# Performance work log

Measured on AMD Instinct MI355X. Metric: run time of the kernel, lower is better.

Reference implementation:

```python
import jax, jax.numpy as jnp
import numpy as np

D_MODEL = 512
N_HEADS = 8
D_HEAD = D_MODEL // N_HEADS
B = 8
N = 1024
EPS = 1e-5  # torch LayerNorm default


def setup_inputs() -> dict:
    key = jax.random.key(0)
    ks = jax.random.split(key, 12)
    x = jax.random.normal(ks[0], (B, N, D_MODEL), dtype=jnp.float32)
    adj = (jax.random.uniform(ks[1], (B, N, N)) < 0.05).astype(jnp.float32)
    s = 1.0 / np.sqrt(D_MODEL)
    def lin(kw, kb):
        W = jax.random.uniform(kw, (D_MODEL, D_MODEL), minval=-s, maxval=s, dtype=jnp.float32)
        b = jax.random.uniform(kb, (D_MODEL,), minval=-s, maxval=s, dtype=jnp.float32)
        return W, b
    Wq, bq = lin(ks[2], ks[3])
    Wk, bk = lin(ks[4], ks[5])
    Wv, bv = lin(ks[6], ks[7])
    Wo, bo = lin(ks[8], ks[9])
    gamma = jnp.ones((D_MODEL,), dtype=jnp.float32)
    beta = jnp.zeros((D_MODEL,), dtype=jnp.float32)
    return {"x": x, "adj": adj, "Wq": Wq, "bq": bq, "Wk": Wk, "bk": bk,
            "Wv": Wv, "bv": bv, "Wo": Wo, "bo": bo, "gamma": gamma, "beta": beta}


def reference(x, adj, Wq, bq, Wk, bk, Wv, bv, Wo, bo, gamma, beta):
    Bsz, n, _ = x.shape
    # QKV projections -> [b, h, n, d]
    def proj(W, b):
        y = x @ W.T + b
        return y.reshape(Bsz, n, N_HEADS, D_HEAD).transpose(0, 2, 1, 3)
    q, k, v = proj(Wq, bq), proj(Wk, bk), proj(Wv, bv)
    scores = jnp.einsum('bhqd,bhkd->bhqk', q, k) / np.sqrt(D_HEAD)
    # adjacency mask + self-loops, broadcast over heads
    mask = (adj + jnp.eye(n, dtype=adj.dtype)[None]) > 0  # [b, n, n]
    scores = jnp.where(mask[:, None], scores, -jnp.inf)
    attn = jax.nn.softmax(scores, axis=-1)  # dropout is identity in eval
    out = jnp.einsum('bhqk,bhkd->bhqd', attn, v)
    out = out.transpose(0, 2, 1, 3).reshape(Bsz, n, D_MODEL)
    out = out @ Wo.T + bo
    # residual + LayerNorm
    h = x + out
    mu = jnp.mean(h, axis=-1, keepdims=True)
    var = jnp.mean(jnp.square(h - mu), axis=-1, keepdims=True)
    return (h - mu) * jax.lax.rsqrt(var + EPS) * gamma + beta
```

## Files before the change

kernel.cpp:

```cpp
#include <hip/hip_runtime.h>

typedef __bf16 bf16;
typedef bf16 bf16x8 __attribute__((ext_vector_type(8)));
typedef bf16 bf16x4 __attribute__((ext_vector_type(4)));
typedef float f32x4 __attribute__((ext_vector_type(4)));
typedef unsigned long long u64;

#define B_SZ 8
#define N_SEQ 1024
#define DMODEL 512
#define N_HEADS 8
#define D_HEAD 64
#define M_ROWS 8192

static constexpr size_t OFF_XB   = 0;
static constexpr size_t OFF_WQKV = (size_t)M_ROWS * DMODEL * 2;
static constexpr size_t OFF_WO   = OFF_WQKV + (size_t)1536 * 512 * 2;
static constexpr size_t OFF_BQKV = OFF_WO + (size_t)512 * 512 * 2;
static constexpr size_t OFF_Q    = OFF_BQKV + 1536 * 4;
static constexpr size_t OFF_K    = OFF_Q + (size_t)64 * 1024 * 64 * 2;
static constexpr size_t OFF_V    = OFF_K + (size_t)64 * 1024 * 64 * 2;
static constexpr size_t OFF_MASK = OFF_V + (size_t)64 * 1024 * 64 * 2;

#define PREP_X_BLK 4096
#define PREP_W_BLK 4102
#define PREP_M_BLK 32768

__device__ __forceinline__ f32x4 mfma16(bf16x8 a, bf16x8 b, f32x4 c) {
  return __builtin_amdgcn_mfma_f32_16x16x32_bf16(a, b, c, 0, 0, 0);
}

__device__ __forceinline__ int sidx(int row, int col) {
  return (row << 6) + (col ^ ((row & 7) << 3));
}

__device__ __forceinline__ void gload16(const void* g, void* l) {
  __builtin_amdgcn_global_load_lds(
      (const __attribute__((address_space(1))) void*)g,
      (__attribute__((address_space(3))) void*)l, 16, 0, 0);
}

__global__ void k_prep(const float* __restrict__ x, const float* __restrict__ adj,
                       const float* __restrict__ Wq, const float* __restrict__ Wk,
                       const float* __restrict__ Wv, const float* __restrict__ Wo,
                       const float* __restrict__ bq, const float* __restrict__ bk,
                       const float* __restrict__ bv,
                       bf16* __restrict__ xb, bf16* __restrict__ wqkv,
                       bf16* __restrict__ wo, float* __restrict__ bqkv,
                       u64* __restrict__ maskb) {
  int b = blockIdx.x;
  if (b < PREP_X_BLK) {
    int i = b * 256 + threadIdx.x;
    float4 v = reinterpret_cast<const float4*>(x)[i];
    bf16x4 o = { (bf16)v.x, (bf16)v.y, (bf16)v.z, (bf16)v.w };
    *reinterpret_cast<bf16x4*>(xb + (size_t)i * 4) = o;
  } else if (b < PREP_X_BLK + PREP_W_BLK) {
    int tid = (b - PREP_X_BLK) * 256 + threadIdx.x;
    if (tid < 1536 * 512) {
      int row = tid >> 9;
      const float* Wsrc = row < 512 ? Wq : row < 1024 ? Wk : Wv;
      wqkv[tid] = (bf16)Wsrc[((row & 511) << 9) | (tid & 511)];
    } else if (tid < 1536 * 512 + 512 * 512) {
      int t = tid - 1536 * 512;
      wo[t] = (bf16)Wo[t];
    } else if (tid < 1536 * 512 + 512 * 512 + 1536) {
      int t = tid - (1536 * 512 + 512 * 512);
      bqkv[t] = t < 512 ? bq[t] : t < 1024 ? bk[t - 512] : bv[t - 1024];
    }
  } else {
    int idx = (b - (PREP_X_BLK + PREP_W_BLK)) * 256 + threadIdx.x;
    int q = (idx >> 10) & 1023, k = idx & 1023;
    bool pred = (adj[idx] > 0.f) || (q == k);
    u64 bal = __ballot(pred);
    if ((threadIdx.x & 63) == 0) maskb[idx >> 6] = bal;
  }
}

__global__ __launch_bounds__(256) void k_gemm(const bf16* __restrict__ A,
    const bf16* __restrict__ W, int ncols, int mode,
    const float* __restrict__ bias, const float* __restrict__ xres,
    bf16* __restrict__ oq, bf16* __restrict__ okk, bf16* __restrict__ ov,
    float* __restrict__ oh) {
  __shared__ bf16 Al[128 * 64];
  __shared__ bf16 Bl[128 * 64];
  int nbx = ncols >> 7;
  int bx = blockIdx.x % nbx, by = blockIdx.x / nbx;
  int m0 = by << 7, n0 = bx << 7;
  int tid = threadIdx.x, lane = tid & 63, w = tid >> 6;
  int wr = (w >> 1) << 6, wc = (w & 1) << 6;
  int lrow = lane & 15, lg = lane >> 4, lko = lg * 8;
  int rl = lane >> 3;
  int csw = ((lane & 7) ^ rl) << 3;

  const bf16* Asrc = A + (size_t)(m0 + w * 32 + rl) * DMODEL + csw;
  const bf16* Wsrc = W + (size_t)(n0 + w * 32 + rl) * DMODEL + csw;
  bf16* Adst = &Al[(w * 4) * 512];
  bf16* Bdst = &Bl[(w * 4) * 512];

  f32x4 acc[4][4];
#pragma unroll
  for (int i = 0; i < 4; i++)
#pragma unroll
    for (int j = 0; j < 4; j++) acc[i][j] = f32x4{0.f, 0.f, 0.f, 0.f};

  for (int k0 = 0; k0 < DMODEL; k0 += 64) {
    __syncthreads();
#pragma unroll
    for (int i = 0; i < 4; i++) {
      gload16(Asrc + k0 + (size_t)i * 8 * DMODEL, Adst + i * 512);
      gload16(Wsrc + k0 + (size_t)i * 8 * DMODEL, Bdst + i * 512);
    }
    __syncthreads();

    bf16x8 afr[4][2], bfr[4][2];
#pragma unroll
    for (int i = 0; i < 4; i++) {
      afr[i][0] = *reinterpret_cast<const bf16x8*>(&Al[sidx(wr + i * 16 + lrow, lko)]);
      afr[i][1] = *reinterpret_cast<const bf16x8*>(&Al[sidx(wr + i * 16 + lrow, 32 + lko)]);
      bfr[i][0] = *reinterpret_cast<const bf16x8*>(&Bl[sidx(wc + i * 16 + lrow, lko)]);
      bfr[i][1] = *reinterpret_cast<const bf16x8*>(&Bl[sidx(wc + i * 16 + lrow, 32 + lko)]);
    }
#pragma unroll
    for (int i = 0; i < 4; i++)
#pragma unroll
      for (int j = 0; j < 4; j++) {
        acc[i][j] = mfma16(afr[i][0], bfr[j][0], acc[i][j]);
        acc[i][j] = mfma16(afr[i][1], bfr[j][1], acc[i][j]);
      }
  }

  int rbase = lg * 4;
  if (mode == 0) {
#pragma unroll
    for (int i = 0; i < 4; i++) {
      int row0 = m0 + wr + i * 16 + rbase;
#pragma unroll
      for (int j = 0; j < 4; j++) {
        int col = n0 + wc + j * 16 + lrow;
        int which = col >> 9, c2 = col & 511, hh = c2 >> 6, dd = c2 & 63;
        float bi = bias[col];
        if (which == 2) {
          int bb = row0 >> 10, nn = row0 & 1023;
          bf16x4 pack;
#pragma unroll
          for (int r = 0; r < 4; r++) pack[r] = (bf16)(acc[i][j][r] + bi);
          *reinterpret_cast<bf16x4*>(
              &ov[(((size_t)bb * N_HEADS + hh) * D_HEAD + dd) * N_SEQ + nn]) = pack;
        } else {
          bf16* dst = which == 0 ? oq : okk;
          float scl = which == 0 ? 0.125f : 1.0f;
#pragma unroll
          for (int r = 0; r < 4; r++) {
            int gm = row0 + r;
            int bb = gm >> 10, nn = gm & 1023;
            dst[(((size_t)bb * N_HEADS + hh) * N_SEQ + nn) * D_HEAD + dd] =
                (bf16)((acc[i][j][r] + bi) * scl);
          }
        }
      }
    }
  } else {
#pragma unroll
    for (int i = 0; i < 4; i++) {
      int row0 = m0 + wr + i * 16 + rbase;
#pragma unroll
      for (int j = 0; j < 4; j++) {
        int col = n0 + wc + j * 16 + lrow;
        float bi = bias[col];
#pragma unroll
        for (int r = 0; r < 4; r++) {
          int gm = row0 + r;
          float y = acc[i][j][r] + bi + xres[(size_t)gm * DMODEL + col];
          oh[(size_t)gm * DMODEL + col] = y;
        }
      }
    }
  }
}

__global__ __launch_bounds__(256) void k_attn(const bf16* __restrict__ Qb,
    const bf16* __restrict__ Kb, const bf16* __restrict__ Vtg,
    const u64* __restrict__ maskb, bf16* __restrict__ attn_out) {
  __shared__ bf16 Kl[2][64 * 64];
  __shared__ bf16 Vt[2][64 * 64];
  __shared__ bf16 Pl[4][16 * 64];

  int bid = blockIdx.x;
  int work = ((bid & 7) << 7) | (bid >> 3);
  int bh = work >> 4, qb = work & 15;
  int bb = bh >> 3, hh = bh & 7;
  int tid = threadIdx.x, lane = tid & 63, w = tid >> 6;
  int lrow = lane & 15, lg = lane >> 4, lko = lg * 8;
  int rl = lane >> 3;
  int csw = ((lane & 7) ^ rl) << 3;
  int q0w = qb * 64 + w * 16;

  const bf16* Qh = Qb + (size_t)bh * N_SEQ * D_HEAD;
  const bf16* Kh = Kb + (size_t)bh * N_SEQ * D_HEAD;
  const bf16* Vh = Vtg + (size_t)bh * D_HEAD * N_SEQ;
  const u64* mrow = maskb + (size_t)bb * N_SEQ * 16;

  const bf16* Ksrc = Kh + (size_t)(w * 16 + rl) * D_HEAD + csw;
  const bf16* Vsrc = Vh + (size_t)(w * 16 + rl) * N_SEQ + csw;

  bf16x8 qf0 = *reinterpret_cast<const bf16x8*>(&Qh[(q0w + lrow) * 64 + lko]);
  bf16x8 qf1 = *reinterpret_cast<const bf16x8*>(&Qh[(q0w + lrow) * 64 + 32 + lko]);

  f32x4 o[4];
  float ls[4] = {0.f, 0.f, 0.f, 0.f};
#pragma unroll
  for (int dt = 0; dt < 4; dt++) o[dt] = f32x4{0.f, 0.f, 0.f, 0.f};

#define STAGE(buf, kt0)                                                     \
  {                                                                         \
    _Pragma("unroll") for (int i = 0; i < 2; i++) {                         \
      gload16(Ksrc + (size_t)(kt0) * 64 + i * 512, &Kl[buf][(w * 2 + i) * 512]); \
      gload16(Vsrc + (size_t)i * 8192 + (kt0), &Vt[buf][(w * 2 + i) * 512]);     \
    }                                                                       \
  }

  STAGE(0, 0);
  __syncthreads();
  int cur = 0;

  for (int kt = 0; kt < 16; kt++) {
    int kt0 = kt << 6;
    u64 mw[4];
#pragma unroll
    for (int r = 0; r < 4; r++) mw[r] = mrow[(size_t)(q0w + lg * 4 + r) * 16 + kt];

    if (kt < 15) STAGE(cur ^ 1, kt0 + 64);

    f32x4 sc[4];
#pragma unroll
    for (int t = 0; t < 4; t++) {
      bf16x8 kf0 = *reinterpret_cast<const bf16x8*>(&Kl[cur][sidx(t * 16 + lrow, lko)]);
      bf16x8 kf1 = *reinterpret_cast<const bf16x8*>(&Kl[cur][sidx(t * 16 + lrow, 32 + lko)]);
      sc[t] = f32x4{0.f, 0.f, 0.f, 0.f};
      sc[t] = mfma16(qf0, kf0, sc[t]);
      sc[t] = mfma16(qf1, kf1, sc[t]);
    }

#pragma unroll
    for (int r = 0; r < 4; r++) {
#pragma unroll
      for (int t = 0; t < 4; t++) {
        bool bit = (mw[r] >> (t * 16 + lrow)) & 1ull;
        float pv = bit ? __expf(sc[t][r]) : 0.f;
        ls[r] += pv;
        Pl[w][sidx(lg * 4 + r, t * 16 + lrow)] = (bf16)pv;
      }
    }

    bf16x8 pf0 = *reinterpret_cast<const bf16x8*>(&Pl[w][sidx(lrow, lko)]);
    bf16x8 pf1 = *reinterpret_cast<const bf16x8*>(&Pl[w][sidx(lrow, 32 + lko)]);
#pragma unroll
    for (int dt = 0; dt < 4; dt++) {
      bf16x8 vf0 = *reinterpret_cast<const bf16x8*>(&Vt[cur][sidx(dt * 16 + lrow, lko)]);
      bf16x8 vf1 = *reinterpret_cast<const bf16x8*>(&Vt[cur][sidx(dt * 16 + lrow, 32 + lko)]);
      o[dt] = mfma16(pf0, vf0, o[dt]);
      o[dt] = mfma16(pf1, vf1, o[dt]);
    }

    __syncthreads();
    cur ^= 1;
  }

#pragma unroll
  for (int r = 0; r < 4; r++) {
    ls[r] += __shfl_xor(ls[r], 1);
    ls[r] += __shfl_xor(ls[r], 2);
    ls[r] += __shfl_xor(ls[r], 4);
    ls[r] += __shfl_xor(ls[r], 8);
  }

#pragma unroll
  for (int dt = 0; dt < 4; dt++) {
    int gc = hh * 64 + dt * 16 + lrow;
#pragma unroll
    for (int r = 0; r < 4; r++) {
      int gq = q0w + lg * 4 + r;
      float val = o[dt][r] / ls[r];
      attn_out[((size_t)(bb * N_SEQ + gq)) * DMODEL + gc] = (bf16)val;
    }
  }
#undef STAGE
}

__global__ __launch_bounds__(256) void k_ln(const float* __restrict__ hbuf,
    const float* __restrict__ gamma, const float* __restrict__ beta,
    float* __restrict__ out) {
  int row = blockIdx.x, tid = threadIdx.x;
  const float* hr = hbuf + (size_t)row * DMODEL;
  float2 v = reinterpret_cast<const float2*>(hr)[tid];
  float s = v.x + v.y, ss = v.x * v.x + v.y * v.y;
#pragma unroll
  for (int off = 1; off < 64; off <<= 1) {
    s += __shfl_xor(s, off);
    ss += __shfl_xor(ss, off);
  }
  __shared__ float as_[4], ass_[4];
  int w = tid >> 6;
  if ((tid & 63) == 0) { as_[w] = s; ass_[w] = ss; }
  __syncthreads();
  s = as_[0] + as_[1] + as_[2] + as_[3];
  ss = ass_[0] + ass_[1] + ass_[2] + ass_[3];
  float mu = s * (1.f / 512.f);
  float var = ss * (1.f / 512.f) - mu * mu;
  float rstd = rsqrtf(var + 1e-5f);
  float2 g = reinterpret_cast<const float2*>(gamma)[tid];
  float2 bt = reinterpret_cast<const float2*>(beta)[tid];
  float2 o;
  o.x = (v.x - mu) * rstd * g.x + bt.x;
  o.y = (v.y - mu) * rstd * g.y + bt.y;
  reinterpret_cast<float2*>(out + (size_t)row * DMODEL)[tid] = o;
}

extern "C" void kernel_launch(void* const* d_in, const int* in_sizes, int n_in,
                              void* d_out, int out_size, void* d_ws, size_t ws_size,
                              hipStream_t stream) {
  const float* x     = (const float*)d_in[0];
  const float* adj   = (const float*)d_in[1];
  const float* Wq    = (const float*)d_in[2];
  const float* bq    = (const float*)d_in[3];
  const float* Wk    = (const float*)d_in[4];
  const float* bk    = (const float*)d_in[5];
  const float* Wv    = (const float*)d_in[6];
  const float* bv    = (const float*)d_in[7];
  const float* Wo    = (const float*)d_in[8];
  const float* bo    = (const float*)d_in[9];
  const float* gamma = (const float*)d_in[10];
  const float* beta  = (const float*)d_in[11];

  char* ws = (char*)d_ws;
  bf16* xb    = (bf16*)(ws + OFF_XB);
  bf16* wqkv  = (bf16*)(ws + OFF_WQKV);
  bf16* wo    = (bf16*)(ws + OFF_WO);
  float* bqkv = (float*)(ws + OFF_BQKV);
  bf16* Qb    = (bf16*)(ws + OFF_Q);
  bf16* Kb    = (bf16*)(ws + OFF_K);
  bf16* Vb    = (bf16*)(ws + OFF_V);
  u64* maskb  = (u64*)(ws + OFF_MASK);
  bf16* attn  = xb;
  float* hbuf = (float*)(ws + OFF_Q);
  float* out  = (float*)d_out;

  k_prep<<<dim3(PREP_X_BLK + PREP_W_BLK + PREP_M_BLK), dim3(256), 0, stream>>>(
      x, adj, Wq, Wk, Wv, Wo, bq, bk, bv, xb, wqkv, wo, bqkv, maskb);

  k_gemm<<<dim3((M_ROWS / 128) * (1536 / 128)), dim3(256), 0, stream>>>(
      xb, wqkv, 1536, 0, bqkv, nullptr, Qb, Kb, Vb, nullptr);

  k_attn<<<dim3(1024), dim3(256), 0, stream>>>(Qb, Kb, Vb, maskb, attn);

  k_gemm<<<dim3((M_ROWS / 128) * (512 / 128)), dim3(256), 0, stream>>>(
      attn, wo, 512, 1, bo, x, nullptr, nullptr, nullptr, hbuf);

  k_ln<<<dim3(M_ROWS), dim3(256), 0, stream>>>(hbuf, gamma, beta, out);
}
```

Baseline: 113.0 us.

## Double attention query tile per warp, use exp2 scaling, store residual sum in bf16

Each attention warp now handles 32 query rows instead of 16, so every K/V tile staged in shared memory feeds twice as many MFMAs, and the grid is halved. Q is prescaled by log2(e)/8 so the softmax can use exp2f instead of __expf. The residual-plus-projection buffer passed to LayerNorm is now written in bf16 instead of fp32, cutting that round trip's memory traffic at some cost in precision. The larger per-warp tile raises register pressure, and the launch bound asks for two blocks per CU.

Result: slower. 116.3 us (+2.9%).

```diff
diff --git a/kernel.cpp b/kernel.cpp
--- a/kernel.cpp
+++ b/kernel.cpp
@@ -3,6 +3,7 @@
 typedef __bf16 bf16;
 typedef bf16 bf16x8 __attribute__((ext_vector_type(8)));
 typedef bf16 bf16x4 __attribute__((ext_vector_type(4)));
+typedef bf16 bf16x2 __attribute__((ext_vector_type(2)));
 typedef float f32x4 __attribute__((ext_vector_type(4)));
 typedef unsigned long long u64;
 
@@ -12,6 +13,8 @@
 #define N_HEADS 8
 #define D_HEAD 64
 #define M_ROWS 8192
+
+#define QSCALE 0.18033688011112042f
 
 static constexpr size_t OFF_XB   = 0;
 static constexpr size_t OFF_WQKV = (size_t)M_ROWS * DMODEL * 2;
@@ -80,7 +83,7 @@
     const bf16* __restrict__ W, int ncols, int mode,
     const float* __restrict__ bias, const float* __restrict__ xres,
     bf16* __restrict__ oq, bf16* __restrict__ okk, bf16* __restrict__ ov,
-    float* __restrict__ oh) {
+    bf16* __restrict__ oh) {
   __shared__ bf16 Al[128 * 64];
   __shared__ bf16 Bl[128 * 64];
   int nbx = ncols >> 7;
@@ -148,7 +151,7 @@
               &ov[(((size_t)bb * N_HEADS + hh) * D_HEAD + dd) * N_SEQ + nn]) = pack;
         } else {
           bf16* dst = which == 0 ? oq : okk;
-          float scl = which == 0 ? 0.125f : 1.0f;
+          float scl = which == 0 ? QSCALE : 1.0f;
 #pragma unroll
           for (int r = 0; r < 4; r++) {
             int gm = row0 + r;
@@ -171,29 +174,29 @@
         for (int r = 0; r < 4; r++) {
           int gm = row0 + r;
           float y = acc[i][j][r] + bi + xres[(size_t)gm * DMODEL + col];
-          oh[(size_t)gm * DMODEL + col] = y;
+          oh[(size_t)gm * DMODEL + col] = (bf16)y;
         }
       }
     }
   }
 }
 
-__global__ __launch_bounds__(256) void k_attn(const bf16* __restrict__ Qb,
+__global__ __launch_bounds__(256, 2) void k_attn(const bf16* __restrict__ Qb,
     const bf16* __restrict__ Kb, const bf16* __restrict__ Vtg,
     const u64* __restrict__ maskb, bf16* __restrict__ attn_out) {
   __shared__ bf16 Kl[2][64 * 64];
   __shared__ bf16 Vt[2][64 * 64];
-  __shared__ bf16 Pl[4][16 * 64];
+  __shared__ bf16 Pl[4][32 * 64];
 
   int bid = blockIdx.x;
-  int work = ((bid & 7) << 7) | (bid >> 3);
-  int bh = work >> 4, qb = work & 15;
+  int work = ((bid & 7) << 6) | (bid >> 3);
+  int bh = work >> 3, qb = work & 7;
   int bb = bh >> 3, hh = bh & 7;
   int tid = threadIdx.x, lane = tid & 63, w = tid >> 6;
   int lrow = lane & 15, lg = lane >> 4, lko = lg * 8;
   int rl = lane >> 3;
   int csw = ((lane & 7) ^ rl) << 3;
-  int q0w = qb * 64 + w * 16;
+  int q0w = qb * 128 + w * 32;
 
   const bf16* Qh = Qb + (size_t)bh * N_SEQ * D_HEAD;
   const bf16* Kh = Kb + (size_t)bh * N_SEQ * D_HEAD;
@@ -203,13 +206,22 @@
   const bf16* Ksrc = Kh + (size_t)(w * 16 + rl) * D_HEAD + csw;
   const bf16* Vsrc = Vh + (size_t)(w * 16 + rl) * N_SEQ + csw;
 
-  bf16x8 qf0 = *reinterpret_cast<const bf16x8*>(&Qh[(q0w + lrow) * 64 + lko]);
-  bf16x8 qf1 = *reinterpret_cast<const bf16x8*>(&Qh[(q0w + lrow) * 64 + 32 + lko]);
-
-  f32x4 o[4];
-  float ls[4] = {0.f, 0.f, 0.f, 0.f};
-#pragma unroll
-  for (int dt = 0; dt < 4; dt++) o[dt] = f32x4{0.f, 0.f, 0.f, 0.f};
+  bf16x8 qf[2][2];
+#pragma unroll
+  for (int s = 0; s < 2; s++) {
+    qf[s][0] = *reinterpret_cast<const bf16x8*>(&Qh[(q0w + s * 16 + lrow) * 64 + lko]);
+    qf[s][1] = *reinterpret_cast<const bf16x8*>(&Qh[(q0w + s * 16 + lrow) * 64 + 32 + lko]);
+  }
+
+  f32x4 o[2][4];
+  float ls[2][4];
+#pragma unroll
+  for (int s = 0; s < 2; s++)
+#pragma unroll
+    for (int t = 0; t < 4; t++) {
+      o[s][t] = f32x4{0.f, 0.f, 0.f, 0.f};
+      ls[s][t] = 0.f;
+    }
 
 #define STAGE(buf, kt0)                                                     \
   {                                                                         \
@@ -225,41 +237,56 @@
 
   for (int kt = 0; kt < 16; kt++) {
     int kt0 = kt << 6;
-    u64 mw[4];
-#pragma unroll
-    for (int r = 0; r < 4; r++) mw[r] = mrow[(size_t)(q0w + lg * 4 + r) * 16 + kt];
+    u64 mw[2][4];
+#pragma unroll
+    for (int s = 0; s < 2; s++)
+#pragma unroll
+      for (int r = 0; r < 4; r++)
+        mw[s][r] = mrow[(size_t)(q0w + s * 16 + lg * 4 + r) * 16 + kt];
 
     if (kt < 15) STAGE(cur ^ 1, kt0 + 64);
 
-    f32x4 sc[4];
+    f32x4 sc[2][4];
 #pragma unroll
     for (int t = 0; t < 4; t++) {
       bf16x8 kf0 = *reinterpret_cast<const bf16x8*>(&Kl[cur][sidx(t * 16 + lrow, lko)]);
       bf16x8 kf1 = *reinterpret_cast<const bf16x8*>(&Kl[cur][sidx(t * 16 + lrow, 32 + lko)]);
-      sc[t] = f32x4{0.f, 0.f, 0.f, 0.f};
-      sc[t] = mfma16(qf0, kf0, sc[t]);
-      sc[t] = mfma16(qf1, kf1, sc[t]);
-    }
-
-#pragma unroll
-    for (int r = 0; r < 4; r++) {
-#pragma unroll
-      for (int t = 0; t < 4; t++) {
-        bool bit = (mw[r] >> (t * 16 + lrow)) & 1ull;
-        float pv = bit ? __expf(sc[t][r]) : 0.f;
-        ls[r] += pv;
-        Pl[w][sidx(lg * 4 + r, t * 16 + lrow)] = (bf16)pv;
-      }
-    }
-
-    bf16x8 pf0 = *reinterpret_cast<const bf16x8*>(&Pl[w][sidx(lrow, lko)]);
-    bf16x8 pf1 = *reinterpret_cast<const bf16x8*>(&Pl[w][sidx(lrow, 32 + lko)]);
+#pragma unroll
+      for (int s = 0; s < 2; s++) {
+        sc[s][t] = f32x4{0.f, 0.f, 0.f, 0.f};
+        sc[s][t] = mfma16(qf[s][0], kf0, sc[s][t]);
+        sc[s][t] = mfma16(qf[s][1], kf1, sc[s][t]);
+      }
+    }
+
+#pragma unroll
+    for (int s = 0; s < 2; s++)
+#pragma unroll
+      for (int r = 0; r < 4; r++) {
+#pragma unroll
+        for (int t = 0; t < 4; t++) {
+          bool bit = (mw[s][r] >> (t * 16 + lrow)) & 1ull;
+          float pv = bit ? exp2f(sc[s][t][r]) : 0.f;
+          ls[s][r] += pv;
+          Pl[w][sidx(s * 16 + lg * 4 + r, t * 16 + lrow)] = (bf16)pv;
+        }
+      }
+
+    bf16x8 pf[2][2];
+#pragma unroll
+    for (int s = 0; s < 2; s++) {
+      pf[s][0] = *reinterpret_cast<const bf16x8*>(&Pl[w][sidx(s * 16 + lrow, lko)]);
+      pf[s][1] = *reinterpret_cast<const bf16x8*>(&Pl[w][sidx(s * 16 + lrow, 32 + lko)]);
+    }
 #pragma unroll
     for (int dt = 0; dt < 4; dt++) {
       bf16x8 vf0 = *reinterpret_cast<const bf16x8*>(&Vt[cur][sidx(dt * 16 + lrow, lko)]);
       bf16x8 vf1 = *reinterpret_cast<const bf16x8*>(&Vt[cur][sidx(dt * 16 + lrow, 32 + lko)]);
-      o[dt] = mfma16(pf0, vf0, o[dt]);
-      o[dt] = mfma16(pf1, vf1, o[dt]);
+#pragma unroll
+      for (int s = 0; s < 2; s++) {
+        o[s][dt] = mfma16(pf[s][0], vf0, o[s][dt]);
+        o[s][dt] = mfma16(pf[s][1], vf1, o[s][dt]);
+      }
     }
 
     __syncthreads();
@@ -267,33 +294,37 @@
   }
 
 #pragma unroll
-  for (int r = 0; r < 4; r++) {
-    ls[r] += __shfl_xor(ls[r], 1);
-    ls[r] += __shfl_xor(ls[r], 2);
-    ls[r] += __shfl_xor(ls[r], 4);
-    ls[r] += __shfl_xor(ls[r], 8);
-  }
-
-#pragma unroll
-  for (int dt = 0; dt < 4; dt++) {
-    int gc = hh * 64 + dt * 16 + lrow;
+  for (int s = 0; s < 2; s++)
 #pragma unroll
     for (int r = 0; r < 4; r++) {
-      int gq = q0w + lg * 4 + r;
-      float val = o[dt][r] / ls[r];
-      attn_out[((size_t)(bb * N_SEQ + gq)) * DMODEL + gc] = (bf16)val;
-    }
-  }
+      ls[s][r] += __shfl_xor(ls[s][r], 1);
+      ls[s][r] += __shfl_xor(ls[s][r], 2);
+      ls[s][r] += __shfl_xor(ls[s][r], 4);
+      ls[s][r] += __shfl_xor(ls[s][r], 8);
+    }
+
+#pragma unroll
+  for (int s = 0; s < 2; s++)
+#pragma unroll
+    for (int dt = 0; dt < 4; dt++) {
+      int gc = hh * 64 + dt * 16 + lrow;
+#pragma unroll
+      for (int r = 0; r < 4; r++) {
+        int gq = q0w + s * 16 + lg * 4 + r;
+        float val = o[s][dt][r] / ls[s][r];
+        attn_out[((size_t)(bb * N_SEQ + gq)) * DMODEL + gc] = (bf16)val;
+      }
+    }
 #undef STAGE
 }
 
-__global__ __launch_bounds__(256) void k_ln(const float* __restrict__ hbuf,
+__global__ __launch_bounds__(256) void k_ln(const bf16* __restrict__ hb,
     const float* __restrict__ gamma, const float* __restrict__ beta,
     float* __restrict__ out) {
   int row = blockIdx.x, tid = threadIdx.x;
-  const float* hr = hbuf + (size_t)row * DMODEL;
-  float2 v = reinterpret_cast<const float2*>(hr)[tid];
-  float s = v.x + v.y, ss = v.x * v.x + v.y * v.y;
+  bf16x2 v2 = *reinterpret_cast<const bf16x2*>(hb + (size_t)row * DMODEL + tid * 2);
+  float vx = (float)v2[0], vy = (float)v2[1];
+  float s = vx + vy, ss = vx * vx + vy * vy;
 #pragma unroll
   for (int off = 1; off < 64; off <<= 1) {
     s += __shfl_xor(s, off);
@@ -311,8 +342,8 @@
   float2 g = reinterpret_cast<const float2*>(gamma)[tid];
   float2 bt = reinterpret_cast<const float2*>(beta)[tid];
   float2 o;
-  o.x = (v.x - mu) * rstd * g.x + bt.x;
-  o.y = (v.y - mu) * rstd * g.y + bt.y;
+  o.x = (vx - mu) * rstd * g.x + bt.x;
+  o.y = (vy - mu) * rstd * g.y + bt.y;
   reinterpret_cast<float2*>(out + (size_t)row * DMODEL)[tid] = o;
 }
 
@@ -342,7 +373,7 @@
   bf16* Vb    = (bf16*)(ws + OFF_V);
   u64* maskb  = (u64*)(ws + OFF_MASK);
   bf16* attn  = xb;
-  float* hbuf = (float*)(ws + OFF_Q);
+  bf16* hb    = (bf16*)(ws + OFF_Q);
   float* out  = (float*)d_out;
 
   k_prep<<<dim3(PREP_X_BLK + PREP_W_BLK + PREP_M_BLK), dim3(256), 0, stream>>>(
@@ -351,10 +382,10 @@
   k_gemm<<<dim3((M_ROWS / 128) * (1536 / 128)), dim3(256), 0, stream>>>(
       xb, wqkv, 1536, 0, bqkv, nullptr, Qb, Kb, Vb, nullptr);
 
-  k_attn<<<dim3(1024), dim3(256), 0, stream>>>(Qb, Kb, Vb, maskb, attn);
+  k_attn<<<dim3(512), dim3(256), 0, stream>>>(Qb, Kb, Vb, maskb, attn);
 
   k_gemm<<<dim3((M_ROWS / 128) * (512 / 128)), dim3(256), 0, stream>>>(
-      attn, wo, 512, 1, bo, x, nullptr, nullptr, nullptr, hbuf);
-
-  k_ln<<<dim3(M_ROWS), dim3(256), 0, stream>>>(hbuf, gamma, beta, out);
-}
+      attn, wo, 512, 1, bo, x, nullptr, nullptr, nullptr, hb);
+
+  k_ln<<<dim3(M_ROWS), dim3(256), 0, stream>>>(hb, gamma, beta, out);
+}
```

## Keep P in registers via transposed QK^T, use exp2, store residual as bf16

Applied to the files above, without the earlier changes.

The attention kernel now computes S^T by swapping the MFMA operands. Each lane's score fragment can then feed the P·V MFMA directly from registers, so the shared-memory P buffer, its writes and its readback go away. Softmax uses exp2 with log2(e) folded into the Q scale. Each lane now loads one mask word instead of four, the row-sum reduction needs fewer shuffles, and output stores are vectorised. The residual h buffer between the output GEMM and LayerNorm is stored as bf16 instead of fp32 to halve that traffic, at some precision cost in LayerNorm statistics. Launch bounds are also set for 4 blocks per SM.

Result: no change. 113.4 us (+0.3%).

```diff
diff --git a/kernel.cpp b/kernel.cpp
--- a/kernel.cpp
+++ b/kernel.cpp
@@ -3,6 +3,7 @@
 typedef __bf16 bf16;
 typedef bf16 bf16x8 __attribute__((ext_vector_type(8)));
 typedef bf16 bf16x4 __attribute__((ext_vector_type(4)));
+typedef bf16 bf16x2 __attribute__((ext_vector_type(2)));
 typedef float f32x4 __attribute__((ext_vector_type(4)));
 typedef unsigned long long u64;
 
@@ -12,6 +13,8 @@
 #define N_HEADS 8
 #define D_HEAD 64
 #define M_ROWS 8192
+
+#define QSCALE 0.18033688011112042f
 
 static constexpr size_t OFF_XB   = 0;
 static constexpr size_t OFF_WQKV = (size_t)M_ROWS * DMODEL * 2;
@@ -80,7 +83,7 @@
     const bf16* __restrict__ W, int ncols, int mode,
     const float* __restrict__ bias, const float* __restrict__ xres,
     bf16* __restrict__ oq, bf16* __restrict__ okk, bf16* __restrict__ ov,
-    float* __restrict__ oh) {
+    bf16* __restrict__ oh) {
   __shared__ bf16 Al[128 * 64];
   __shared__ bf16 Bl[128 * 64];
   int nbx = ncols >> 7;
@@ -148,7 +151,7 @@
               &ov[(((size_t)bb * N_HEADS + hh) * D_HEAD + dd) * N_SEQ + nn]) = pack;
         } else {
           bf16* dst = which == 0 ? oq : okk;
-          float scl = which == 0 ? 0.125f : 1.0f;
+          float scl = which == 0 ? QSCALE : 1.0f;
 #pragma unroll
           for (int r = 0; r < 4; r++) {
             int gm = row0 + r;
@@ -171,26 +174,25 @@
         for (int r = 0; r < 4; r++) {
           int gm = row0 + r;
           float y = acc[i][j][r] + bi + xres[(size_t)gm * DMODEL + col];
-          oh[(size_t)gm * DMODEL + col] = y;
+          oh[(size_t)gm * DMODEL + col] = (bf16)y;
         }
       }
     }
   }
 }
 
-__global__ __launch_bounds__(256) void k_attn(const bf16* __restrict__ Qb,
+__global__ __launch_bounds__(256, 4) void k_attn(const bf16* __restrict__ Qb,
     const bf16* __restrict__ Kb, const bf16* __restrict__ Vtg,
     const u64* __restrict__ maskb, bf16* __restrict__ attn_out) {
   __shared__ bf16 Kl[2][64 * 64];
   __shared__ bf16 Vt[2][64 * 64];
-  __shared__ bf16 Pl[4][16 * 64];
 
   int bid = blockIdx.x;
   int work = ((bid & 7) << 7) | (bid >> 3);
   int bh = work >> 4, qb = work & 15;
   int bb = bh >> 3, hh = bh & 7;
   int tid = threadIdx.x, lane = tid & 63, w = tid >> 6;
-  int lrow = lane & 15, lg = lane >> 4, lko = lg * 8;
+  int lrow = lane & 15, lg = lane >> 4;
   int rl = lane >> 3;
   int csw = ((lane & 7) ^ rl) << 3;
   int q0w = qb * 64 + w * 16;
@@ -203,13 +205,13 @@
   const bf16* Ksrc = Kh + (size_t)(w * 16 + rl) * D_HEAD + csw;
   const bf16* Vsrc = Vh + (size_t)(w * 16 + rl) * N_SEQ + csw;
 
-  bf16x8 qf0 = *reinterpret_cast<const bf16x8*>(&Qh[(q0w + lrow) * 64 + lko]);
-  bf16x8 qf1 = *reinterpret_cast<const bf16x8*>(&Qh[(q0w + lrow) * 64 + 32 + lko]);
+  bf16x8 qf0 = *reinterpret_cast<const bf16x8*>(&Qh[(q0w + lrow) * 64 + lg * 8]);
+  bf16x8 qf1 = *reinterpret_cast<const bf16x8*>(&Qh[(q0w + lrow) * 64 + 32 + lg * 8]);
 
   f32x4 o[4];
-  float ls[4] = {0.f, 0.f, 0.f, 0.f};
-#pragma unroll
-  for (int dt = 0; dt < 4; dt++) o[dt] = f32x4{0.f, 0.f, 0.f, 0.f};
+#pragma unroll
+  for (int d = 0; d < 4; d++) o[d] = f32x4{0.f, 0.f, 0.f, 0.f};
+  float ls = 0.f;
 
 #define STAGE(buf, kt0)                                                     \
   {                                                                         \
@@ -225,75 +227,73 @@
 
   for (int kt = 0; kt < 16; kt++) {
     int kt0 = kt << 6;
-    u64 mw[4];
-#pragma unroll
-    for (int r = 0; r < 4; r++) mw[r] = mrow[(size_t)(q0w + lg * 4 + r) * 16 + kt];
+    u64 mw = mrow[(size_t)(q0w + lrow) * 16 + kt];
 
     if (kt < 15) STAGE(cur ^ 1, kt0 + 64);
 
     f32x4 sc[4];
 #pragma unroll
     for (int t = 0; t < 4; t++) {
-      bf16x8 kf0 = *reinterpret_cast<const bf16x8*>(&Kl[cur][sidx(t * 16 + lrow, lko)]);
-      bf16x8 kf1 = *reinterpret_cast<const bf16x8*>(&Kl[cur][sidx(t * 16 + lrow, 32 + lko)]);
+      bf16x8 kf0 = *reinterpret_cast<const bf16x8*>(&Kl[cur][sidx(t * 16 + lrow, lg * 8)]);
+      bf16x8 kf1 = *reinterpret_cast<const bf16x8*>(&Kl[cur][sidx(t * 16 + lrow, 32 + lg * 8)]);
       sc[t] = f32x4{0.f, 0.f, 0.f, 0.f};
-      sc[t] = mfma16(qf0, kf0, sc[t]);
-      sc[t] = mfma16(qf1, kf1, sc[t]);
-    }
-
-#pragma unroll
-    for (int r = 0; r < 4; r++) {
-#pragma unroll
-      for (int t = 0; t < 4; t++) {
-        bool bit = (mw[r] >> (t * 16 + lrow)) & 1ull;
-        float pv = bit ? __expf(sc[t][r]) : 0.f;
-        ls[r] += pv;
-        Pl[w][sidx(lg * 4 + r, t * 16 + lrow)] = (bf16)pv;
-      }
-    }
-
-    bf16x8 pf0 = *reinterpret_cast<const bf16x8*>(&Pl[w][sidx(lrow, lko)]);
-    bf16x8 pf1 = *reinterpret_cast<const bf16x8*>(&Pl[w][sidx(lrow, 32 + lko)]);
-#pragma unroll
-    for (int dt = 0; dt < 4; dt++) {
-      bf16x8 vf0 = *reinterpret_cast<const bf16x8*>(&Vt[cur][sidx(dt * 16 + lrow, lko)]);
-      bf16x8 vf1 = *reinterpret_cast<const bf16x8*>(&Vt[cur][sidx(dt * 16 + lrow, 32 + lko)]);
-      o[dt] = mfma16(pf0, vf0, o[dt]);
-      o[dt] = mfma16(pf1, vf1, o[dt]);
+      sc[t] = mfma16(kf0, qf0, sc[t]);
+      sc[t] = mfma16(kf1, qf1, sc[t]);
+    }
+
+    bf16x8 pa[2];
+#pragma unroll
+    for (int m = 0; m < 2; m++) {
+#pragma unroll
+      for (int j = 0; j < 8; j++) {
+        int t = 2 * m + (j >> 2), r = j & 3;
+        bool bit = (mw >> (t * 16 + lg * 4 + r)) & 1ull;
+        float pv = bit ? exp2f(sc[t][r]) : 0.f;
+        ls += pv;
+        pa[m][j] = (bf16)pv;
+      }
+    }
+
+#pragma unroll
+    for (int d = 0; d < 4; d++) {
+#pragma unroll
+      for (int m = 0; m < 2; m++) {
+        bf16x4 va = *reinterpret_cast<const bf16x4*>(
+            &Vt[cur][sidx(d * 16 + lrow, m * 32 + lg * 4)]);
+        bf16x4 vb = *reinterpret_cast<const bf16x4*>(
+            &Vt[cur][sidx(d * 16 + lrow, m * 32 + 16 + lg * 4)]);
+        bf16x8 vf = {va[0], va[1], va[2], va[3], vb[0], vb[1], vb[2], vb[3]};
+        o[d] = mfma16(vf, pa[m], o[d]);
+      }
     }
 
     __syncthreads();
     cur ^= 1;
   }
 
-#pragma unroll
-  for (int r = 0; r < 4; r++) {
-    ls[r] += __shfl_xor(ls[r], 1);
-    ls[r] += __shfl_xor(ls[r], 2);
-    ls[r] += __shfl_xor(ls[r], 4);
-    ls[r] += __shfl_xor(ls[r], 8);
-  }
-
-#pragma unroll
-  for (int dt = 0; dt < 4; dt++) {
-    int gc = hh * 64 + dt * 16 + lrow;
-#pragma unroll
-    for (int r = 0; r < 4; r++) {
-      int gq = q0w + lg * 4 + r;
-      float val = o[dt][r] / ls[r];
-      attn_out[((size_t)(bb * N_SEQ + gq)) * DMODEL + gc] = (bf16)val;
-    }
+  ls += __shfl_xor(ls, 16);
+  ls += __shfl_xor(ls, 32);
+  float inv = 1.f / ls;
+
+  int gq = q0w + lrow;
+#pragma unroll
+  for (int d = 0; d < 4; d++) {
+    bf16x4 pk;
+#pragma unroll
+    for (int r = 0; r < 4; r++) pk[r] = (bf16)(o[d][r] * inv);
+    *reinterpret_cast<bf16x4*>(
+        &attn_out[((size_t)(bb * N_SEQ + gq)) * DMODEL + hh * 64 + d * 16 + lg * 4]) = pk;
   }
 #undef STAGE
 }
 
-__global__ __launch_bounds__(256) void k_ln(const float* __restrict__ hbuf,
+__global__ __launch_bounds__(256) void k_ln(const bf16* __restrict__ hb,
     const float* __restrict__ gamma, const float* __restrict__ beta,
     float* __restrict__ out) {
   int row = blockIdx.x, tid = threadIdx.x;
-  const float* hr = hbuf + (size_t)row * DMODEL;
-  float2 v = reinterpret_cast<const float2*>(hr)[tid];
-  float s = v.x + v.y, ss = v.x * v.x + v.y * v.y;
+  bf16x2 v2 = *reinterpret_cast<const bf16x2*>(hb + (size_t)row * DMODEL + tid * 2);
+  float vx = (float)v2[0], vy = (float)v2[1];
+  float s = vx + vy, ss = vx * vx + vy * vy;
 #pragma unroll
   for (int off = 1; off < 64; off <<= 1) {
     s += __shfl_xor(s, off);
@@ -311,8 +311,8 @@
   float2 g = reinterpret_cast<const float2*>(gamma)[tid];
   float2 bt = reinterpret_cast<const float2*>(beta)[tid];
   float2 o;
-  o.x = (v.x - mu) * rstd * g.x + bt.x;
-  o.y = (v.y - mu) * rstd * g.y + bt.y;
+  o.x = (vx - mu) * rstd * g.x + bt.x;
+  o.y = (vy - mu) * rstd * g.y + bt.y;
   reinterpret_cast<float2*>(out + (size_t)row * DMODEL)[tid] = o;
 }
 
@@ -342,7 +342,7 @@
   bf16* Vb    = (bf16*)(ws + OFF_V);
   u64* maskb  = (u64*)(ws + OFF_MASK);
   bf16* attn  = xb;
-  float* hbuf = (float*)(ws + OFF_Q);
+  bf16* hb    = (bf16*)(ws + OFF_Q);
   float* out  = (float*)d_out;
 
   k_prep<<<dim3(PREP_X_BLK + PREP_W_BLK + PREP_M_BLK), dim3(256), 0, stream>>>(
@@ -354,7 +354,7 @@
   k_attn<<<dim3(1024), dim3(256), 0, stream>>>(Qb, Kb, Vb, maskb, attn);
 
   k_gemm<<<dim3((M_ROWS / 128) * (512 / 128)), dim3(256), 0, stream>>>(
-      attn, wo, 512, 1, bo, x, nullptr, nullptr, nullptr, hbuf);
-
-  k_ln<<<dim3(M_ROWS), dim3(256), 0, stream>>>(hbuf, gamma, beta, out);
-}
+      attn, wo, 512, 1, bo, x, nullptr, nullptr, nullptr, hb);
+
+  k_ln<<<dim3(M_ROWS), dim3(256), 0, stream>>>(hb, gamma, beta, out);
+}
```
